# Kernel optimization log

Hardware: AMD Instinct MI355X
Metric: run time of the kernel (lower is better)

## Reference

```python
import jax, jax.numpy as jnp
import numpy as np

B, S, D = 2, 2048, 1024
H = 16
HD = D // H  # 64


def _xavier(key, shape):
    fan_in, fan_out = shape[1], shape[0]
    a = jnp.sqrt(6.0 / (fan_in + fan_out))
    return jax.random.uniform(key, shape, jnp.float32, -a, a)


def setup_inputs() -> dict:
    key = jax.random.key(0)
    ks = jax.random.split(key, 7)
    xq = jax.random.normal(ks[0], (B, S, D), jnp.float32)
    xv = jax.random.normal(ks[1], (B, S, D), jnp.float32)
    xk = jax.random.normal(ks[2], (B, S, D), jnp.float32)
    Wq = _xavier(ks[3], (D, D)); bq = jnp.zeros((D,), jnp.float32)
    Wk = _xavier(ks[4], (D, D)); bk = jnp.zeros((D,), jnp.float32)
    Wv = _xavier(ks[5], (D, D)); bv = jnp.zeros((D,), jnp.float32)
    Wo = _xavier(ks[6], (D, D)); bo = jnp.zeros((D,), jnp.float32)
    return {"xq": xq, "xv": xv, "xk": xk,
            "Wq": Wq, "bq": bq, "Wk": Wk, "bk": bk,
            "Wv": Wv, "bv": bv, "Wo": Wo, "bo": bo}


def reference(xq, xv, xk, Wq, bq, Wk, bk, Wv, bv, Wo, bo):
    # Q/K/V projections (torch Linear: x @ W.T + b), split heads -> [B,H,S,HD]
    q = (xq @ Wq.T + bq).reshape(B, S, H, HD).transpose(0, 2, 1, 3)
    k = (xk @ Wk.T + bk).reshape(B, S, H, HD).transpose(0, 2, 1, 3)
    v = (xv @ Wv.T + bv).reshape(B, S, H, HD).transpose(0, 2, 1, 3)
    # scaled dot-product attention, no mask
    logits = jnp.einsum('bhqd,bhkd->bhqk', q, k) / jnp.sqrt(jnp.float32(HD))
    attn = jax.nn.softmax(logits, axis=-1)
    values = jnp.einsum('bhqk,bhkd->bhqd', attn, v)
    values = values.transpose(0, 2, 1, 3).reshape(B, S, D)
    return values @ Wo.T + bo
```

## Files before the change

### kernel.cpp

```cpp
#include <hip/hip_runtime.h>

typedef __bf16 bf16x8 __attribute__((ext_vector_type(8)));
typedef float f32x4 __attribute__((ext_vector_type(4)));
typedef __attribute__((address_space(1))) const unsigned char ga_t;
typedef __attribute__((address_space(3))) unsigned char la_t;

static __device__ __forceinline__ unsigned short f2b(float f) {
  union { float f; unsigned int i; } c; c.f = f;
  unsigned int r = c.i + 0x7FFFu + ((c.i >> 16) & 1u);
  return (unsigned short)(r >> 16);
}
static __device__ __forceinline__ unsigned int pack2(float a, float b) {
  return (unsigned int)f2b(a) | ((unsigned int)f2b(b) << 16);
}
static __device__ __forceinline__ int4 ld8f_cvt(const float* __restrict__ p) {
  float4 a = *(const float4*)p;
  float4 b = *(const float4*)(p + 4);
  unsigned short u[8];
  u[0] = f2b(a.x); u[1] = f2b(a.y); u[2] = f2b(a.z); u[3] = f2b(a.w);
  u[4] = f2b(b.x); u[5] = f2b(b.y); u[6] = f2b(b.z); u[7] = f2b(b.w);
  return *(int4*)u;
}
static __device__ __forceinline__ void glds16(const unsigned short* g, unsigned short* l) {
  __builtin_amdgcn_global_load_lds((ga_t*)g, (la_t*)l, 16, 0, 0);
}

__global__ __launch_bounds__(256)
void cvt_z(const float* __restrict__ s0, const float* __restrict__ s1,
           const float* __restrict__ s2, const float* __restrict__ s3,
           unsigned short* d0, unsigned short* d1,
           unsigned short* d2, unsigned short* d3, int n8) {
  const int z = blockIdx.y;
  const float* s = z == 0 ? s0 : z == 1 ? s1 : z == 2 ? s2 : s3;
  unsigned short* d = z == 0 ? d0 : z == 1 ? d1 : z == 2 ? d2 : d3;
  int idx = blockIdx.x * 256 + threadIdx.x;
  if (idx < n8) *(int4*)(d + (size_t)idx * 8) = ld8f_cvt(s + (size_t)idx * 8);
}

static __device__ __forceinline__ void gemm_core(
    const unsigned short* __restrict__ A, const unsigned short* __restrict__ W,
    unsigned short* sA, unsigned short* sB, f32x4 acc[4][4],
    int K, int m0, int n0) {
  const int tid = threadIdx.x;
  const int wave = tid >> 6, lane = tid & 63, quad = lane >> 4, l16 = lane & 15;
  const int wrow = (wave >> 1) * 64, wcol = (wave & 1) * 64;
  const int r = tid >> 2, c8 = (tid & 3) * 8;

  const unsigned short* gA0 = A + (size_t)(m0 + r) * K + c8;
  const unsigned short* gA1 = gA0 + (size_t)64 * K;
  const unsigned short* gB0 = W + (size_t)(n0 + r) * K + c8;
  const unsigned short* gB1 = gB0 + (size_t)64 * K;
  unsigned short* lA0 = sA + tid * 8;
  unsigned short* lA1 = lA0 + 2048;
  unsigned short* lB0 = sB + tid * 8;
  unsigned short* lB1 = lB0 + 2048;

  for (int k0 = 0; k0 < K; k0 += 32) {
    __syncthreads();
    glds16(gA0 + k0, lA0);
    glds16(gA1 + k0, lA1);
    glds16(gB0 + k0, lB0);
    glds16(gB1 + k0, lB1);
    __syncthreads();

    bf16x8 af[4], bfv[4];
#pragma unroll
    for (int i = 0; i < 4; ++i)
      af[i] = *(const bf16x8*)(&sA[(wrow + i * 16 + l16) * 32 + quad * 8]);
#pragma unroll
    for (int j = 0; j < 4; ++j)
      bfv[j] = *(const bf16x8*)(&sB[(wcol + j * 16 + l16) * 32 + quad * 8]);
#pragma unroll
    for (int i = 0; i < 4; ++i)
#pragma unroll
      for (int j = 0; j < 4; ++j)
        acc[i][j] = __builtin_amdgcn_mfma_f32_16x16x32_bf16(af[i], bfv[j], acc[i][j], 0, 0, 0);
  }
}

__global__ __launch_bounds__(256, 3)
void gemm_qkv(const unsigned short* __restrict__ A0p, const unsigned short* __restrict__ A1p,
              const unsigned short* __restrict__ A2p,
              const unsigned short* __restrict__ W0p, const unsigned short* __restrict__ W1p,
              const unsigned short* __restrict__ W2p,
              const float* __restrict__ b0p, const float* __restrict__ b1p,
              const float* __restrict__ b2p,
              unsigned short* __restrict__ C0p, unsigned short* __restrict__ C1p,
              unsigned short* __restrict__ C2p,
              int M, int N, int K, int zbase) {
  __shared__ __align__(16) unsigned short smem[8192];
  const int z = blockIdx.z + zbase;
  const unsigned short* A = z == 0 ? A0p : z == 1 ? A1p : A2p;
  const unsigned short* W = z == 0 ? W0p : z == 1 ? W1p : W2p;
  const float* bias = z == 0 ? b0p : z == 1 ? b1p : b2p;

  const int tid = threadIdx.x;
  const int wave = tid >> 6, lane = tid & 63, quad = lane >> 4, l16 = lane & 15;
  const int m0 = blockIdx.x * 128, n0 = blockIdx.y * 128;
  const int wrow = (wave >> 1) * 64, wcol = (wave & 1) * 64;

  f32x4 acc[4][4];
#pragma unroll
  for (int i = 0; i < 4; ++i)
#pragma unroll
    for (int j = 0; j < 4; ++j) acc[i][j] = (f32x4){0.f, 0.f, 0.f, 0.f};

  gemm_core(A, W, smem, smem + 4096, acc, K, m0, n0);

  if (z < 2) {
    unsigned short* C = z == 0 ? C0p : C1p;
#pragma unroll
    for (int j = 0; j < 4; ++j) {
      const int col = n0 + wcol + j * 16 + l16;
      const float bv = bias[col];
#pragma unroll
      for (int i = 0; i < 4; ++i)
#pragma unroll
        for (int r = 0; r < 4; ++r) {
          const int row = m0 + wrow + i * 16 + quad * 4 + r;
          C[(size_t)row * N + col] = f2b(acc[i][j][r] + bv);
        }
    }
  } else {
    __syncthreads();
    unsigned short* sT = smem + wave * 1152;
#pragma unroll
    for (int j = 0; j < 4; ++j) {
      const float bv = bias[n0 + wcol + j * 16 + l16];
#pragma unroll
      for (int i = 0; i < 4; ++i) {
        uint2 pk;
        pk.x = pack2(acc[i][j][0] + bv, acc[i][j][1] + bv);
        pk.y = pack2(acc[i][j][2] + bv, acc[i][j][3] + bv);
        *(uint2*)(&sT[l16 * 72 + i * 16 + quad * 4]) = pk;
      }
#pragma unroll
      for (int t = 0; t < 2; ++t) {
        const int nl = lane >> 2;
        const int colh = (lane & 3) * 8 + t * 32;
        int4 v = *(const int4*)(&sT[nl * 72 + colh]);
        *(int4*)(&C2p[(size_t)(n0 + wcol + j * 16 + nl) * M + m0 + wrow + colh]) = v;
      }
    }
  }
}

__global__ __launch_bounds__(256, 3)
void gemm_out(const unsigned short* __restrict__ A, const unsigned short* __restrict__ W,
              const float* __restrict__ bias, float* __restrict__ C,
              int M, int N, int K) {
  __shared__ __align__(16) unsigned short smem[8192];
  const int tid = threadIdx.x;
  const int wave = tid >> 6, lane = tid & 63, quad = lane >> 4, l16 = lane & 15;
  const int m0 = blockIdx.x * 128, n0 = blockIdx.y * 128;
  const int wrow = (wave >> 1) * 64, wcol = (wave & 1) * 64;

  f32x4 acc[4][4];
#pragma unroll
  for (int i = 0; i < 4; ++i)
#pragma unroll
    for (int j = 0; j < 4; ++j) acc[i][j] = (f32x4){0.f, 0.f, 0.f, 0.f};

  gemm_core(A, W, smem, smem + 4096, acc, K, m0, n0);

#pragma unroll
  for (int j = 0; j < 4; ++j) {
    const int col = n0 + wcol + j * 16 + l16;
    const float bv = bias[col];
#pragma unroll
    for (int i = 0; i < 4; ++i)
#pragma unroll
      for (int r = 0; r < 4; ++r) {
        const int row = m0 + wrow + i * 16 + quad * 4 + r;
        C[(size_t)row * N + col] = acc[i][j][r] + bv;
      }
  }
}

#define SEQ 2048
#define DMODEL 1024

__global__ __launch_bounds__(256, 2)
void attn_fused(const unsigned short* __restrict__ Q,
                const unsigned short* __restrict__ Km,
                const unsigned short* __restrict__ Vt,
                unsigned short* __restrict__ O) {
  __shared__ __align__(16) unsigned short sK[2][4096];
  __shared__ __align__(16) unsigned short sVt[2][4096];
  __shared__ __align__(16) unsigned short sPb[4][2304];

  const int tid = threadIdx.x;
  const int wave = tid >> 6, lane = tid & 63, quad = lane >> 4, l16 = lane & 15;
  const int qt = blockIdx.x;
  const int bh = blockIdx.y;
  const int b = bh >> 4, h = bh & 15;
  const size_t qrow0 = (size_t)b * SEQ + qt * 128;
  const size_t kvrow0 = (size_t)b * SEQ;
  const int hcol = h * 64;
  const int bofs = b * SEQ;
  const int qw = wave * 32;

  bf16x8 qa[2][2];
#pragma unroll
  for (int qi = 0; qi < 2; ++qi)
#pragma unroll
    for (int ks = 0; ks < 2; ++ks) {
      int4 v = *(const int4*)(&Q[(qrow0 + qw + qi * 16 + l16) * DMODEL + hcol + ks * 32 + quad * 8]);
      qa[qi][ks] = *(bf16x8*)&v;
    }

  unsigned short* sP = sPb[wave];

  f32x4 acc[2][4];
#pragma unroll
  for (int qi = 0; qi < 2; ++qi)
#pragma unroll
    for (int hg = 0; hg < 4; ++hg) acc[qi][hg] = (f32x4){0.f, 0.f, 0.f, 0.f};
  float lsum[2] = {0.f, 0.f};

  const float SCL = 0.18033688011112042f;

  const unsigned short* gK0 = Km + (kvrow0 + wave * 16 + l16) * DMODEL + hcol + quad * 8;
  const unsigned short* gV0 = Vt + (size_t)(hcol + wave * 16 + l16) * 4096 + bofs + quad * 8;
  unsigned short* lK0 = &sK[0][wave * 1024 + lane * 8];
  unsigned short* lV0 = &sVt[0][wave * 1024 + lane * 8];

#pragma unroll
  for (int half = 0; half < 2; ++half) {
    glds16(gK0 + half * 32, lK0 + half * 512);
    glds16(gV0 + half * 32, lV0 + half * 512);
  }

  for (int kt = 0; kt < SEQ; kt += 64) {
    const int pb = (kt >> 6) & 1;
    __syncthreads();

    const int ktn = (kt + 64 < SEQ) ? kt + 64 : kt;
    unsigned short* lKn = lK0 + (pb ^ 1) * 4096;
    unsigned short* lVn = lV0 + (pb ^ 1) * 4096;
#pragma unroll
    for (int half = 0; half < 2; ++half) {
      glds16(gK0 + (size_t)ktn * DMODEL + half * 32, lKn + half * 512);
      glds16(gV0 + ktn + half * 32, lVn + half * 512);
    }

    f32x4 s[2][4];
#pragma unroll
    for (int qi = 0; qi < 2; ++qi)
#pragma unroll
      for (int kg = 0; kg < 4; ++kg) s[qi][kg] = (f32x4){0.f, 0.f, 0.f, 0.f};
#pragma unroll
    for (int kg = 0; kg < 4; ++kg) {
      bf16x8 kb0 = *(const bf16x8*)(&sK[pb][(kg * 2 + 0) * 512 + lane * 8]);
      bf16x8 kb1 = *(const bf16x8*)(&sK[pb][(kg * 2 + 1) * 512 + lane * 8]);
#pragma unroll
      for (int qi = 0; qi < 2; ++qi) {
        s[qi][kg] = __builtin_amdgcn_mfma_f32_16x16x32_bf16(kb0, qa[qi][0], s[qi][kg], 0, 0, 0);
        s[qi][kg] = __builtin_amdgcn_mfma_f32_16x16x32_bf16(kb1, qa[qi][1], s[qi][kg], 0, 0, 0);
      }
    }

#pragma unroll
    for (int qi = 0; qi < 2; ++qi)
#pragma unroll
      for (int kg = 0; kg < 4; ++kg) {
        float p0 = __builtin_amdgcn_exp2f(s[qi][kg][0] * SCL);
        float p1 = __builtin_amdgcn_exp2f(s[qi][kg][1] * SCL);
        float p2 = __builtin_amdgcn_exp2f(s[qi][kg][2] * SCL);
        float p3 = __builtin_amdgcn_exp2f(s[qi][kg][3] * SCL);
        lsum[qi] += (p0 + p1) + (p2 + p3);
        uint2 pk; pk.x = pack2(p0, p1); pk.y = pack2(p2, p3);
        *(uint2*)(&sP[(qi * 16 + l16) * 72 + kg * 16 + quad * 4]) = pk;
      }

#pragma unroll
    for (int ks = 0; ks < 2; ++ks) {
      bf16x8 pa[2], vb[4];
#pragma unroll
      for (int qi = 0; qi < 2; ++qi)
        pa[qi] = *(const bf16x8*)(&sP[(qi * 16 + l16) * 72 + ks * 32 + quad * 8]);
#pragma unroll
      for (int hg = 0; hg < 4; ++hg)
        vb[hg] = *(const bf16x8*)(&sVt[pb][(hg * 2 + ks) * 512 + lane * 8]);
#pragma unroll
      for (int qi = 0; qi < 2; ++qi)
#pragma unroll
        for (int hg = 0; hg < 4; ++hg)
          acc[qi][hg] = __builtin_amdgcn_mfma_f32_16x16x32_bf16(pa[qi], vb[hg], acc[qi][hg], 0, 0, 0);
    }
  }

#pragma unroll
  for (int qi = 0; qi < 2; ++qi) {
    float v = lsum[qi];
    v += __shfl_xor(v, 16, 64);
    v += __shfl_xor(v, 32, 64);
    lsum[qi] = v;
  }
  float linv[2][4];
#pragma unroll
  for (int qi = 0; qi < 2; ++qi)
#pragma unroll
    for (int r = 0; r < 4; ++r)
      linv[qi][r] = 1.0f / __shfl(lsum[qi], quad * 4 + r, 64);

#pragma unroll
  for (int qi = 0; qi < 2; ++qi)
#pragma unroll
    for (int hg = 0; hg < 4; ++hg)
#pragma unroll
      for (int r = 0; r < 4; ++r) {
        const size_t row = qrow0 + qw + qi * 16 + quad * 4 + r;
        O[row * DMODEL + hcol + hg * 16 + l16] = f2b(acc[qi][hg][r] * linv[qi][r]);
      }
}

extern "C" void kernel_launch(void* const* d_in, const int* in_sizes, int n_in,
                              void* d_out, int out_size, void* d_ws, size_t ws_size,
                              hipStream_t stream) {
  const float* xq = (const float*)d_in[0];
  const float* xv = (const float*)d_in[1];
  const float* xk = (const float*)d_in[2];
  const float* Wq = (const float*)d_in[3];
  const float* bq = (const float*)d_in[4];
  const float* Wk = (const float*)d_in[5];
  const float* bk = (const float*)d_in[6];
  const float* Wv = (const float*)d_in[7];
  const float* bv = (const float*)d_in[8];
  const float* Wo = (const float*)d_in[9];
  const float* bo = (const float*)d_in[10];
  float* out = (float*)d_out;

  const int S = 2048, D = 1024, M = 4096;
  const size_t MD = (size_t)M * D, DD = (size_t)D * D;
  unsigned short* P = (unsigned short*)d_ws;
  dim3 bb(256);
  dim3 gg(M / 128, D / 128);

  const size_t need = (3 * MD + 4 * DD + 3 * MD) * 2;
  if (ws_size >= need) {
    unsigned short* Ab = P;
    unsigned short* Wb = Ab + 3 * MD;
    unsigned short* Qw = Wb + 4 * DD;
    unsigned short* Kw = Qw + MD;
    unsigned short* Vtw = Kw + MD;
    unsigned short* Ao = Ab;

    cvt_z<<<dim3((int)(MD / 8 / 256), 3), bb, 0, stream>>>(
        xq, xk, xv, xq, Ab, Ab + MD, Ab + 2 * MD, Ab, (int)(MD / 8));
    cvt_z<<<dim3((int)(DD / 8 / 256), 4), bb, 0, stream>>>(
        Wq, Wk, Wv, Wo, Wb, Wb + DD, Wb + 2 * DD, Wb + 3 * DD, (int)(DD / 8));
    gemm_qkv<<<dim3(M / 128, D / 128, 3), bb, 0, stream>>>(
        Ab, Ab + MD, Ab + 2 * MD, Wb, Wb + DD, Wb + 2 * DD,
        bq, bk, bv, Qw, Kw, Vtw, M, D, D, 0);
    attn_fused<<<dim3(S / 128, 32), bb, 0, stream>>>(Qw, Kw, Vtw, Ao);
    gemm_out<<<gg, bb, 0, stream>>>(Ao, Wb + 3 * DD, bo, out, M, D, D);
  } else {
    unsigned short* Ab = P;
    unsigned short* Wb = Ab + MD;
    unsigned short* Qw = Wb + DD;
    unsigned short* Kw = Qw + MD;
    unsigned short* Vtw = Kw + MD;
    unsigned short* Ao = Ab;
    const int an = (int)(MD / 8), wn = (int)(DD / 8);

    cvt_z<<<dim3(an / 256, 1), bb, 0, stream>>>(xq, xq, xq, xq, Ab, Ab, Ab, Ab, an);
    cvt_z<<<dim3(wn / 256, 1), bb, 0, stream>>>(Wq, Wq, Wq, Wq, Wb, Wb, Wb, Wb, wn);
    gemm_qkv<<<dim3(M / 128, D / 128, 1), bb, 0, stream>>>(
        Ab, Ab, Ab, Wb, Wb, Wb, bq, bq, bq, Qw, Qw, Qw, M, D, D, 0);

    cvt_z<<<dim3(an / 256, 1), bb, 0, stream>>>(xk, xk, xk, xk, Ab, Ab, Ab, Ab, an);
    cvt_z<<<dim3(wn / 256, 1), bb, 0, stream>>>(Wk, Wk, Wk, Wk, Wb, Wb, Wb, Wb, wn);
    gemm_qkv<<<dim3(M / 128, D / 128, 1), bb, 0, stream>>>(
        Ab, Ab, Ab, Wb, Wb, Wb, bk, bk, bk, Kw, Kw, Kw, M, D, D, 0);

    cvt_z<<<dim3(an / 256, 1), bb, 0, stream>>>(xv, xv, xv, xv, Ab, Ab, Ab, Ab, an);
    cvt_z<<<dim3(wn / 256, 1), bb, 0, stream>>>(Wv, Wv, Wv, Wv, Wb, Wb, Wb, Wb, wn);
    gemm_qkv<<<dim3(M / 128, D / 128, 1), bb, 0, stream>>>(
        Ab, Ab, Ab, Wb, Wb, Wb, bv, bv, bv, Vtw, Vtw, Vtw, M, D, D, 2);

    attn_fused<<<dim3(S / 128, 32), bb, 0, stream>>>(Qw, Kw, Vtw, Ao);

    cvt_z<<<dim3(wn / 256, 1), bb, 0, stream>>>(Wo, Wo, Wo, Wo, Wb, Wb, Wb, Wb, wn);
    gemm_out<<<gg, bb, 0, stream>>>(Ao, Wb, bo, out, M, D, D);
  }
}
```

Baseline: 242.2 us.

## Fold softmax scale into Q, compute row sums via MFMA, use hardware bf16 pack

The softmax scale (1/sqrt(d)·log2e) is now applied in the Q projection epilogue, which removes a multiply per score in the attention inner loop. Row sums of P are computed with an extra MFMA against a ones vector instead of scalar adds and cross-lane shuffles. The bf16 pair conversion now uses the v_cvt_pk_bf16_f32 instruction in place of manual rounding. Rounding Q after scaling and summing bf16-rounded probabilities slightly changes numerics. The extra MFMA adds matrix-core work per tile.

Measured after the change: 232.6 us. 1.04x faster.

```diff
diff --git a/kernel.cpp b/kernel.cpp
--- a/kernel.cpp
+++ b/kernel.cpp
@@ -11,15 +11,17 @@
   return (unsigned short)(r >> 16);
 }
 static __device__ __forceinline__ unsigned int pack2(float a, float b) {
-  return (unsigned int)f2b(a) | ((unsigned int)f2b(b) << 16);
+  unsigned int r;
+  asm("v_cvt_pk_bf16_f32 %0, %1, %2" : "=v"(r) : "v"(a), "v"(b));
+  return r;
 }
 static __device__ __forceinline__ int4 ld8f_cvt(const float* __restrict__ p) {
   float4 a = *(const float4*)p;
   float4 b = *(const float4*)(p + 4);
-  unsigned short u[8];
-  u[0] = f2b(a.x); u[1] = f2b(a.y); u[2] = f2b(a.z); u[3] = f2b(a.w);
-  u[4] = f2b(b.x); u[5] = f2b(b.y); u[6] = f2b(b.z); u[7] = f2b(b.w);
-  return *(int4*)u;
+  uint4 u;
+  u.x = pack2(a.x, a.y); u.y = pack2(a.z, a.w);
+  u.z = pack2(b.x, b.y); u.w = pack2(b.z, b.w);
+  return *(int4*)&u;
 }
 static __device__ __forceinline__ void glds16(const unsigned short* g, unsigned short* l) {
   __builtin_amdgcn_global_load_lds((ga_t*)g, (la_t*)l, 16, 0, 0);
@@ -87,7 +89,7 @@
               const float* __restrict__ b2p,
               unsigned short* __restrict__ C0p, unsigned short* __restrict__ C1p,
               unsigned short* __restrict__ C2p,
-              int M, int N, int K, int zbase) {
+              int M, int N, int K, int zbase, float q0scale) {
   __shared__ __align__(16) unsigned short smem[8192];
   const int z = blockIdx.z + zbase;
   const unsigned short* A = z == 0 ? A0p : z == 1 ? A1p : A2p;
@@ -109,6 +111,7 @@
 
   if (z < 2) {
     unsigned short* C = z == 0 ? C0p : C1p;
+    const float qs = (z == 0) ? q0scale : 1.0f;
 #pragma unroll
     for (int j = 0; j < 4; ++j) {
       const int col = n0 + wcol + j * 16 + l16;
@@ -118,7 +121,7 @@
 #pragma unroll
         for (int r = 0; r < 4; ++r) {
           const int row = m0 + wrow + i * 16 + quad * 4 + r;
-          C[(size_t)row * N + col] = f2b(acc[i][j][r] + bv);
+          C[(size_t)row * N + col] = f2b((acc[i][j][r] + bv) * qs);
         }
     }
   } else {
@@ -209,16 +212,19 @@
       qa[qi][ks] = *(bf16x8*)&v;
     }
 
+  bf16x8 ones;
+#pragma unroll
+  for (int i = 0; i < 8; ++i) ones[i] = (__bf16)1.0f;
+
   unsigned short* sP = sPb[wave];
 
-  f32x4 acc[2][4];
-#pragma unroll
-  for (int qi = 0; qi < 2; ++qi)
+  f32x4 acc[2][4], lacc[2];
+#pragma unroll
+  for (int qi = 0; qi < 2; ++qi) {
+    lacc[qi] = (f32x4){0.f, 0.f, 0.f, 0.f};
 #pragma unroll
     for (int hg = 0; hg < 4; ++hg) acc[qi][hg] = (f32x4){0.f, 0.f, 0.f, 0.f};
-  float lsum[2] = {0.f, 0.f};
-
-  const float SCL = 0.18033688011112042f;
+  }
 
   const unsigned short* gK0 = Km + (kvrow0 + wave * 16 + l16) * DMODEL + hcol + quad * 8;
   const unsigned short* gV0 = Vt + (size_t)(hcol + wave * 16 + l16) * 4096 + bofs + quad * 8;
@@ -264,11 +270,10 @@
     for (int qi = 0; qi < 2; ++qi)
 #pragma unroll
       for (int kg = 0; kg < 4; ++kg) {
-        float p0 = __builtin_amdgcn_exp2f(s[qi][kg][0] * SCL);
-        float p1 = __builtin_amdgcn_exp2f(s[qi][kg][1] * SCL);
-        float p2 = __builtin_amdgcn_exp2f(s[qi][kg][2] * SCL);
-        float p3 = __builtin_amdgcn_exp2f(s[qi][kg][3] * SCL);
-        lsum[qi] += (p0 + p1) + (p2 + p3);
+        float p0 = __builtin_amdgcn_exp2f(s[qi][kg][0]);
+        float p1 = __builtin_amdgcn_exp2f(s[qi][kg][1]);
+        float p2 = __builtin_amdgcn_exp2f(s[qi][kg][2]);
+        float p3 = __builtin_amdgcn_exp2f(s[qi][kg][3]);
         uint2 pk; pk.x = pack2(p0, p1); pk.y = pack2(p2, p3);
         *(uint2*)(&sP[(qi * 16 + l16) * 72 + kg * 16 + quad * 4]) = pk;
       }
@@ -283,36 +288,25 @@
       for (int hg = 0; hg < 4; ++hg)
         vb[hg] = *(const bf16x8*)(&sVt[pb][(hg * 2 + ks) * 512 + lane * 8]);
 #pragma unroll
-      for (int qi = 0; qi < 2; ++qi)
+      for (int qi = 0; qi < 2; ++qi) {
 #pragma unroll
         for (int hg = 0; hg < 4; ++hg)
           acc[qi][hg] = __builtin_amdgcn_mfma_f32_16x16x32_bf16(pa[qi], vb[hg], acc[qi][hg], 0, 0, 0);
-    }
-  }
-
-#pragma unroll
-  for (int qi = 0; qi < 2; ++qi) {
-    float v = lsum[qi];
-    v += __shfl_xor(v, 16, 64);
-    v += __shfl_xor(v, 32, 64);
-    lsum[qi] = v;
-  }
-  float linv[2][4];
+        lacc[qi] = __builtin_amdgcn_mfma_f32_16x16x32_bf16(pa[qi], ones, lacc[qi], 0, 0, 0);
+      }
+    }
+  }
+
 #pragma unroll
   for (int qi = 0; qi < 2; ++qi)
 #pragma unroll
-    for (int r = 0; r < 4; ++r)
-      linv[qi][r] = 1.0f / __shfl(lsum[qi], quad * 4 + r, 64);
-
-#pragma unroll
-  for (int qi = 0; qi < 2; ++qi)
-#pragma unroll
-    for (int hg = 0; hg < 4; ++hg)
-#pragma unroll
-      for (int r = 0; r < 4; ++r) {
-        const size_t row = qrow0 + qw + qi * 16 + quad * 4 + r;
-        O[row * DMODEL + hcol + hg * 16 + l16] = f2b(acc[qi][hg][r] * linv[qi][r]);
-      }
+    for (int r = 0; r < 4; ++r) {
+      const float linv = 1.0f / lacc[qi][r];
+      const size_t row = qrow0 + qw + qi * 16 + quad * 4 + r;
+#pragma unroll
+      for (int hg = 0; hg < 4; ++hg)
+        O[row * DMODEL + hcol + hg * 16 + l16] = f2b(acc[qi][hg][r] * linv);
+    }
 }
 
 extern "C" void kernel_launch(void* const* d_in, const int* in_sizes, int n_in,
@@ -333,6 +327,7 @@
 
   const int S = 2048, D = 1024, M = 4096;
   const size_t MD = (size_t)M * D, DD = (size_t)D * D;
+  const float SCL = 0.18033688011112042f;
   unsigned short* P = (unsigned short*)d_ws;
   dim3 bb(256);
   dim3 gg(M / 128, D / 128);
@@ -352,7 +347,7 @@
         Wq, Wk, Wv, Wo, Wb, Wb + DD, Wb + 2 * DD, Wb + 3 * DD, (int)(DD / 8));
     gemm_qkv<<<dim3(M / 128, D / 128, 3), bb, 0, stream>>>(
         Ab, Ab + MD, Ab + 2 * MD, Wb, Wb + DD, Wb + 2 * DD,
-        bq, bk, bv, Qw, Kw, Vtw, M, D, D, 0);
+        bq, bk, bv, Qw, Kw, Vtw, M, D, D, 0, SCL);
     attn_fused<<<dim3(S / 128, 32), bb, 0, stream>>>(Qw, Kw, Vtw, Ao);
     gemm_out<<<gg, bb, 0, stream>>>(Ao, Wb + 3 * DD, bo, out, M, D, D);
   } else {
@@ -367,17 +362,17 @@
     cvt_z<<<dim3(an / 256, 1), bb, 0, stream>>>(xq, xq, xq, xq, Ab, Ab, Ab, Ab, an);
     cvt_z<<<dim3(wn / 256, 1), bb, 0, stream>>>(Wq, Wq, Wq, Wq, Wb, Wb, Wb, Wb, wn);
     gemm_qkv<<<dim3(M / 128, D / 128, 1), bb, 0, stream>>>(
-        Ab, Ab, Ab, Wb, Wb, Wb, bq, bq, bq, Qw, Qw, Qw, M, D, D, 0);
+        Ab, Ab, Ab, Wb, Wb, Wb, bq, bq, bq, Qw, Qw, Qw, M, D, D, 0, SCL);
 
     cvt_z<<<dim3(an / 256, 1), bb, 0, stream>>>(xk, xk, xk, xk, Ab, Ab, Ab, Ab, an);
     cvt_z<<<dim3(wn / 256, 1), bb, 0, stream>>>(Wk, Wk, Wk, Wk, Wb, Wb, Wb, Wb, wn);
     gemm_qkv<<<dim3(M / 128, D / 128, 1), bb, 0, stream>>>(
-        Ab, Ab, Ab, Wb, Wb, Wb, bk, bk, bk, Kw, Kw, Kw, M, D, D, 0);
+        Ab, Ab, Ab, Wb, Wb, Wb, bk, bk, bk, Kw, Kw, Kw, M, D, D, 0, 1.0f);
 
     cvt_z<<<dim3(an / 256, 1), bb, 0, stream>>>(xv, xv, xv, xv, Ab, Ab, Ab, Ab, an);
     cvt_z<<<dim3(wn / 256, 1), bb, 0, stream>>>(Wv, Wv, Wv, Wv, Wb, Wb, Wb, Wb, wn);
     gemm_qkv<<<dim3(M / 128, D / 128, 1), bb, 0, stream>>>(
-        Ab, Ab, Ab, Wb, Wb, Wb, bv, bv, bv, Vtw, Vtw, Vtw, M, D, D, 2);
+        Ab, Ab, Ab, Wb, Wb, Wb, bv, bv, bv, Vtw, Vtw, Vtw, M, D, D, 2, 1.0f);
 
     attn_fused<<<dim3(S / 128, 32), bb, 0, stream>>>(Qw, Kw, Vtw, Ao);
 
```
